# Kernel tuning notes

Measured on AMD Instinct MI355X. Metric: run time of the kernel, lower is better.

Reference implementation:

```python
import jax, jax.numpy as jnp
import numpy as np

A, B, K, P, STRIDE, ITERS = 32, 32, 3, 4, 2, 3
PSIZE = P * P
EPS = 1e-8


def add_patches(x):
    # x: (b, h, w, A*PSIZE) -> (b*oh*ow, K*K*A, PSIZE)
    b, h, w, c = x.shape
    oh = (h - K) // STRIDE + 1
    ow = (w - K) // STRIDE + 1
    idx = jnp.arange(oh) * STRIDE  # same for w since h == w here
    idx = idx[:, None] + jnp.arange(K)[None, :]          # (oh, K)
    p = x[:, idx]                                        # (b, oh, K, w, c)
    p = p[:, :, :, idx]                                  # (b, oh, K, ow, K, c)
    p = jnp.transpose(p, (0, 1, 3, 2, 4, 5))             # (b, oh, ow, K, K, c)
    p = p.reshape(b * oh * ow, K * K * A, PSIZE)
    return p, oh, ow


def transform_view(p_in, weights):
    # p_in: (N, K*K*A, PSIZE); weights: (K*K*A, B, P, P)
    N = p_in.shape[0]
    x = p_in.reshape(N, K * K * A, P, P)
    # pose matmul per (input capsule i, output type j): x[n,i] @ w[i,j]
    v = jnp.einsum('nipr,ijrq->nijpq', x, weights)       # (N, KKA, B, P, P)
    return v.reshape(N, K * K * A, B, PSIZE)


def squash(p):
    n2 = jnp.sum(p * p, axis=-1, keepdims=True)
    return p * n2 / (1.0 + n2) / jnp.sqrt(n2 + EPS)


def dynamic_routing(v, iters):
    # v: (N, KKA, B, PSIZE); inverted dynamic routing: softmax over input capsules
    N, KKA, Bt, _ = v.shape
    logits = jnp.zeros((N, KKA, Bt, 1), dtype=v.dtype)
    p = None
    for i in range(iters):
        r = jax.nn.softmax(logits, axis=1)               # route over input capsules
        p = squash(jnp.sum(r * v, axis=1, keepdims=True))  # (N,1,B,PSIZE)
        if i < iters - 1:
            logits = logits + jnp.sum(v * p, axis=-1, keepdims=True)
    return p[:, 0]                                       # (N, B, PSIZE)


def setup_inputs() -> dict:
    key = jax.random.key(0)
    k1, k2 = jax.random.split(key)
    x = jax.random.normal(k1, (2, 32, 32, A * PSIZE), dtype=jnp.float32)
    weights = jax.random.normal(k2, (K * K * A, B, P, P), dtype=jnp.float32)
    return {"x": x, "weights": weights}


def reference(x, weights):
    b = x.shape[0]
    p_in, oh, ow = add_patches(x)
    v = transform_view(p_in, weights)                    # (b*oh*ow, KKA, B, PSIZE)
    p_out = dynamic_routing(v, ITERS)                    # (b*oh*ow, B, PSIZE)
    return p_out.reshape(b, oh, ow, B * PSIZE)
```

## Files before the change

kernel.cpp:

```cpp
#include <hip/hip_runtime.h>


#define OH 15
#define OW 15
#define EPS_ 1e-8f

#define XT_ELEMS (2 * 32 * 32 * 512)
#define WT_ELEMS (32 * 5 * 64 * 16)

typedef float v2f __attribute__((ext_vector_type(2)));

__device__ __forceinline__ v2f pfma(float a, v2f b, v2f c) {
    return __builtin_elementwise_fma((v2f){a, a}, b, c);
}
__device__ __forceinline__ float b_lo(unsigned int u) {
    union { unsigned int i; float f; } c; c.i = u << 16; return c.f;
}
__device__ __forceinline__ float b_hi(unsigned int u) {
    union { unsigned int i; float f; } c; c.i = u & 0xFFFF0000u; return c.f;
}
__device__ __forceinline__ unsigned short f2bf(float f) {
    union { float f; unsigned int i; } c; c.f = f;
    return (unsigned short)((c.i + 0x7FFFu + ((c.i >> 16) & 1u)) >> 16);
}

__global__ __launch_bounds__(256) void stage_kernel(
    const float* __restrict__ x, const float* __restrict__ w,
    unsigned short* __restrict__ xt, unsigned short* __restrict__ wt)
{
    const int tid = blockIdx.x * 256 + threadIdx.x;
    if (tid < XT_ELEMS) {
        xt[tid] = f2bf(x[tid]);
    } else {
        const int t2 = tid - XT_ELEMS;
        const int j  = t2 / 5120;
        const int r  = t2 - j * 5120;
        const int k  = r >> 10;
        const int L  = (r >> 4) & 63;
        const int e  = r & 15;
        const int i  = L + 64 * k;
        wt[t2] = (i < 288) ? f2bf(w[(size_t)i * 512 + j * 16 + e])
                           : (unsigned short)0;
    }
}

template <bool PERM>
__global__ __launch_bounds__(64, 3) void convcaps_kernel(
    const void* __restrict__ xp,
    const void* __restrict__ wp_,
    float* __restrict__ out)
{
    const int blk  = blockIdx.x;
    const int n    = blk >> 5;
    const int j    = blk & 31;
    const int lane = threadIdx.x;

    const int batch = n / (OH * OW);
    const int rem   = n - batch * OH * OW;
    const int oy    = rem / OW;
    const int ox    = rem - oy * OW;

    const bool has5 = (lane < 32);

    v2f v[5][8];
    float logit[5] = {0.f, 0.f, 0.f, 0.f, has5 ? 0.f : -1e30f};

#pragma unroll
    for (int k = 0; k < 5; ++k) {
        if (k == 4 && !has5) {
#pragma unroll
            for (int m = 0; m < 8; ++m) v[4][m] = (v2f){0.f, 0.f};
        } else {
            const int i  = lane + 64 * k;
            const int a  = i & 31;
            const int kw = (i >> 5) % 3;
            const int kh = i / 96;
            const int h  = oy * 2 + kh;
            const int wc = ox * 2 + kw;
            const int pixel = (batch * 32 + h) * 32 + wc;

            float xr[16];
            v2f wr2[4][2];
            if (PERM) {
                const uint4* xb = reinterpret_cast<const uint4*>(
                    (const unsigned short*)xp + ((size_t)pixel * 512 + a * 16));
                uint4 u0 = xb[0], u1 = xb[1];
                xr[0]=b_lo(u0.x); xr[1]=b_hi(u0.x); xr[2]=b_lo(u0.y); xr[3]=b_hi(u0.y);
                xr[4]=b_lo(u0.z); xr[5]=b_hi(u0.z); xr[6]=b_lo(u0.w); xr[7]=b_hi(u0.w);
                xr[8]=b_lo(u1.x); xr[9]=b_hi(u1.x); xr[10]=b_lo(u1.y); xr[11]=b_hi(u1.y);
                xr[12]=b_lo(u1.z); xr[13]=b_hi(u1.z); xr[14]=b_lo(u1.w); xr[15]=b_hi(u1.w);
                const uint4* wb = reinterpret_cast<const uint4*>(
                    (const unsigned short*)wp_ + (((size_t)j * 5 + k) * 64 + lane) * 16);
                uint4 q0 = wb[0], q1 = wb[1];
                wr2[0][0] = (v2f){b_lo(q0.x), b_hi(q0.x)};
                wr2[0][1] = (v2f){b_lo(q0.y), b_hi(q0.y)};
                wr2[1][0] = (v2f){b_lo(q0.z), b_hi(q0.z)};
                wr2[1][1] = (v2f){b_lo(q0.w), b_hi(q0.w)};
                wr2[2][0] = (v2f){b_lo(q1.x), b_hi(q1.x)};
                wr2[2][1] = (v2f){b_lo(q1.y), b_hi(q1.y)};
                wr2[3][0] = (v2f){b_lo(q1.z), b_hi(q1.z)};
                wr2[3][1] = (v2f){b_lo(q1.w), b_hi(q1.w)};
            } else {
                const float4* xv = reinterpret_cast<const float4*>(
                    (const float*)xp + ((size_t)pixel * 512 + a * 16));
                float4 x0 = xv[0], x1 = xv[1], x2 = xv[2], x3 = xv[3];
                float t_[16] = { x0.x,x0.y,x0.z,x0.w, x1.x,x1.y,x1.z,x1.w,
                                 x2.x,x2.y,x2.z,x2.w, x3.x,x3.y,x3.z,x3.w };
#pragma unroll
                for (int e = 0; e < 16; ++e) xr[e] = t_[e];
                const float4* wq = reinterpret_cast<const float4*>(
                    (const float*)wp_ + ((size_t)i * 32 + j) * 16);
                float4 w0 = wq[0], w1 = wq[1], w2 = wq[2], w3 = wq[3];
                wr2[0][0]=(v2f){w0.x,w0.y}; wr2[0][1]=(v2f){w0.z,w0.w};
                wr2[1][0]=(v2f){w1.x,w1.y}; wr2[1][1]=(v2f){w1.z,w1.w};
                wr2[2][0]=(v2f){w2.x,w2.y}; wr2[2][1]=(v2f){w2.z,w2.w};
                wr2[3][0]=(v2f){w3.x,w3.y}; wr2[3][1]=(v2f){w3.z,w3.w};
            }

#pragma unroll
            for (int p = 0; p < 4; ++p) {
#pragma unroll
                for (int qq = 0; qq < 2; ++qq) {
                    v2f acc = (v2f){0.f, 0.f};
                    acc = pfma(xr[p*4+0], wr2[0][qq], acc);
                    acc = pfma(xr[p*4+1], wr2[1][qq], acc);
                    acc = pfma(xr[p*4+2], wr2[2][qq], acc);
                    acc = pfma(xr[p*4+3], wr2[3][qq], acc);
                    v[k][p*2+qq] = acc;
                }
            }
        }
    }

#pragma unroll
    for (int it = 0; it < 3; ++it) {
        v2f c2[8];
        float se_loc;
        if (it == 0) {
#pragma unroll
            for (int m = 0; m < 8; ++m)
                c2[m] = v[0][m] + v[1][m] + v[2][m] + v[3][m] + v[4][m];
            se_loc = 0.f;
        } else {
            const float e0 = __expf(logit[0]), e1 = __expf(logit[1]);
            const float e2 = __expf(logit[2]), e3 = __expf(logit[3]);
            const float e4 = __expf(logit[4]);
#pragma unroll
            for (int m = 0; m < 8; ++m)
                c2[m] = pfma(e0, v[0][m],
                        pfma(e1, v[1][m],
                        pfma(e2, v[2][m],
                        pfma(e3, v[3][m],
                        pfma(e4, v[4][m], (v2f){0.f, 0.f})))));
            se_loc = e0 + e1 + e2 + e3 + e4;
        }

        float c[16];
#pragma unroll
        for (int m = 0; m < 8; ++m) { c[2*m] = c2[m].x; c[2*m+1] = c2[m].y; }

        float seR = se_loc;
        float s8[8];
        {
            const bool b = lane & 1;
#pragma unroll
            for (int m = 0; m < 8; ++m) {
                float send = b ? c[2*m]   : c[2*m+1];
                float keep = b ? c[2*m+1] : c[2*m];
                s8[m] = keep + __shfl_xor(send, 1);
            }
            if (it > 0) seR += __shfl_xor(seR, 1);
        }
        float s4[4];
        {
            const bool b = (lane >> 1) & 1;
#pragma unroll
            for (int m = 0; m < 4; ++m) {
                float send = b ? s8[2*m]   : s8[2*m+1];
                float keep = b ? s8[2*m+1] : s8[2*m];
                s4[m] = keep + __shfl_xor(send, 2);
            }
            if (it > 0) seR += __shfl_xor(seR, 2);
        }
        float s2v[2];
        {
            const bool b = (lane >> 2) & 1;
#pragma unroll
            for (int m = 0; m < 2; ++m) {
                float send = b ? s4[2*m]   : s4[2*m+1];
                float keep = b ? s4[2*m+1] : s4[2*m];
                s2v[m] = keep + __shfl_xor(send, 4);
            }
            if (it > 0) seR += __shfl_xor(seR, 4);
        }
        float s1;
        {
            const bool b = (lane >> 3) & 1;
            float send = b ? s2v[0] : s2v[1];
            float keep = b ? s2v[1] : s2v[0];
            s1 = keep + __shfl_xor(send, 8);
            if (it > 0) seR += __shfl_xor(seR, 8);
        }
        s1 += __shfl_xor(s1, 16);  if (it > 0) seR += __shfl_xor(seR, 16);
        s1 += __shfl_xor(s1, 32);  if (it > 0) seR += __shfl_xor(seR, 32);

        const float s = (it == 0) ? s1 * (1.0f / 288.0f) : s1 / seR;

        float t2 = s * s;
        t2 += __shfl_xor(t2, 1);
        t2 += __shfl_xor(t2, 2);
        t2 += __shfl_xor(t2, 4);
        t2 += __shfl_xor(t2, 8);
        const float n2 = t2;
        const float scale = n2 / ((1.0f + n2) * sqrtf(n2 + EPS_));
        const float pval = s * scale;

        if (it < 2) {
            float p[16];
#pragma unroll
            for (int q = 0; q < 16; ++q) p[q] = __shfl(pval, q);
            v2f p2[8];
#pragma unroll
            for (int m = 0; m < 8; ++m) p2[m] = (v2f){p[2*m], p[2*m+1]};
#pragma unroll
            for (int k = 0; k < 5; ++k) {
                v2f acc = (v2f){0.f, 0.f};
#pragma unroll
                for (int m = 0; m < 8; ++m)
                    acc = __builtin_elementwise_fma(v[k][m], p2[m], acc);
                logit[k] += acc.x + acc.y;
            }
        } else {
            if (lane < 16)
                out[(size_t)n * 512 + j * 16 + lane] = pval;
        }
    }
}

extern "C" void kernel_launch(void* const* d_in, const int* in_sizes, int n_in,
                              void* d_out, int out_size, void* d_ws, size_t ws_size,
                              hipStream_t stream) {
    const float* x = (const float*)d_in[0];
    const float* w = (const float*)d_in[1];
    float* out = (float*)d_out;
    const int nblocks = 450 * 32;

    const size_t need = (size_t)(XT_ELEMS + WT_ELEMS) * sizeof(unsigned short);
    if (d_ws != nullptr && ws_size >= need) {
        unsigned short* xt = (unsigned short*)d_ws;
        unsigned short* wt = xt + XT_ELEMS;
        stage_kernel<<<(XT_ELEMS + WT_ELEMS) / 256, 256, 0, stream>>>(x, w, xt, wt);
        convcaps_kernel<true><<<nblocks, 64, 0, stream>>>(xt, wt, out);
    } else {
        convcaps_kernel<false><<<nblocks, 64, 0, stream>>>(x, w, out);
    }
}
```

Before: 86.15 us.

## Stage 3x3 input patch in LDS and share it across four output types

Each block now handles four output capsule types (one per wavefront) for a single output position instead of one, with 256 threads per block. The 9-pixel bf16 input patch is loaded cooperatively into shared memory once and then read from LDS by all four waves, cutting redundant global/L2 reads of x. The iteration-0 sum of votes is also accumulated during the vote computation. This adds a __syncthreads and LDS traffic, and the launch bound of 256 threads with 3 blocks per CU may constrain registers for the large per-thread vote array.

```diff
diff --git a/kernel.cpp b/kernel.cpp
--- a/kernel.cpp
+++ b/kernel.cpp
@@ -45,15 +45,18 @@
 }
 
 template <bool PERM>
-__global__ __launch_bounds__(64, 3) void convcaps_kernel(
+__global__ __launch_bounds__(256, 3) void convcaps_kernel(
     const void* __restrict__ xp,
     const void* __restrict__ wp_,
     float* __restrict__ out)
 {
     const int blk  = blockIdx.x;
-    const int n    = blk >> 5;
-    const int j    = blk & 31;
-    const int lane = threadIdx.x;
+    const int n    = blk >> 3;
+    const int jg   = blk & 7;
+    const int t    = threadIdx.x;
+    const int wv   = t >> 6;
+    const int lane = t & 63;
+    const int j    = jg * 4 + wv;
 
     const int batch = n / (OH * OW);
     const int rem   = n - batch * OH * OW;
@@ -62,7 +65,25 @@
 
     const bool has5 = (lane < 32);
 
+    __shared__ unsigned short xlds[9 * 512];
+
+    if (PERM) {
+        const unsigned short* xt = (const unsigned short*)xp;
+        const int pixbase = (batch * 32 + oy * 2) * 32 + ox * 2;
+        for (int p = wv; p < 9; p += 4) {
+            const int kh = p / 3;
+            const int kw = p - kh * 3;
+            const unsigned short* src =
+                xt + ((size_t)(pixbase + kh * 32 + kw)) * 512 + lane * 8;
+            *(uint4*)&xlds[p * 512 + lane * 8] = *(const uint4*)src;
+        }
+        __syncthreads();
+    }
+
     v2f v[5][8];
+    v2f c2i[8];
+#pragma unroll
+    for (int m = 0; m < 8; ++m) c2i[m] = (v2f){0.f, 0.f};
     float logit[5] = {0.f, 0.f, 0.f, 0.f, has5 ? 0.f : -1e30f};
 
 #pragma unroll
@@ -75,15 +96,12 @@
             const int a  = i & 31;
             const int kw = (i >> 5) % 3;
             const int kh = i / 96;
-            const int h  = oy * 2 + kh;
-            const int wc = ox * 2 + kw;
-            const int pixel = (batch * 32 + h) * 32 + wc;
 
             float xr[16];
             v2f wr2[4][2];
             if (PERM) {
                 const uint4* xb = reinterpret_cast<const uint4*>(
-                    (const unsigned short*)xp + ((size_t)pixel * 512 + a * 16));
+                    xlds + (kh * 3 + kw) * 512 + a * 16);
                 uint4 u0 = xb[0], u1 = xb[1];
                 xr[0]=b_lo(u0.x); xr[1]=b_hi(u0.x); xr[2]=b_lo(u0.y); xr[3]=b_hi(u0.y);
                 xr[4]=b_lo(u0.z); xr[5]=b_hi(u0.z); xr[6]=b_lo(u0.w); xr[7]=b_hi(u0.w);
@@ -101,6 +119,9 @@
                 wr2[3][0] = (v2f){b_lo(q1.z), b_hi(q1.z)};
                 wr2[3][1] = (v2f){b_lo(q1.w), b_hi(q1.w)};
             } else {
+                const int h  = oy * 2 + kh;
+                const int wc = ox * 2 + kw;
+                const int pixel = (batch * 32 + h) * 32 + wc;
                 const float4* xv = reinterpret_cast<const float4*>(
                     (const float*)xp + ((size_t)pixel * 512 + a * 16));
                 float4 x0 = xv[0], x1 = xv[1], x2 = xv[2], x3 = xv[3];
@@ -129,6 +150,8 @@
                     v[k][p*2+qq] = acc;
                 }
             }
+#pragma unroll
+            for (int m = 0; m < 8; ++m) c2i[m] += v[k][m];
         }
     }
 
@@ -138,8 +161,7 @@
         float se_loc;
         if (it == 0) {
 #pragma unroll
-            for (int m = 0; m < 8; ++m)
-                c2[m] = v[0][m] + v[1][m] + v[2][m] + v[3][m] + v[4][m];
+            for (int m = 0; m < 8; ++m) c2[m] = c2i[m];
             se_loc = 0.f;
         } else {
             const float e0 = __expf(logit[0]), e1 = __expf(logit[1]);
@@ -243,15 +265,15 @@
     const float* x = (const float*)d_in[0];
     const float* w = (const float*)d_in[1];
     float* out = (float*)d_out;
-    const int nblocks = 450 * 32;
+    const int nblocks = 450 * 8;
 
     const size_t need = (size_t)(XT_ELEMS + WT_ELEMS) * sizeof(unsigned short);
     if (d_ws != nullptr && ws_size >= need) {
         unsigned short* xt = (unsigned short*)d_ws;
         unsigned short* wt = xt + XT_ELEMS;
         stage_kernel<<<(XT_ELEMS + WT_ELEMS) / 256, 256, 0, stream>>>(x, w, xt, wt);
-        convcaps_kernel<true><<<nblocks, 64, 0, stream>>>(xt, wt, out);
+        convcaps_kernel<true><<<nblocks, 256, 0, stream>>>(xt, wt, out);
     } else {
-        convcaps_kernel<false><<<nblocks, 64, 0, stream>>>(x, w, out);
-    }
-}
+        convcaps_kernel<false><<<nblocks, 256, 0, stream>>>(x, w, out);
+    }
+}
```

Result: slower. 89.71 us (+4.1%).
